# Performance work log

Hardware: AMD Instinct MI355X
Metric: run time of the kernel (lower is better)

## Reference

```python
import jax, jax.numpy as jnp
import numpy as np

GROUPS = 16
EPS_GN = 1e-6
EPS_L2 = 1e-12


def setup_inputs() -> dict:
    key = jax.random.key(0)
    ks = jax.random.split(key, 5)
    B, C, H, W = 8, 256, 64, 64
    s = 0.02
    return {
        "x": jax.random.normal(ks[0], (B, C, H, W), dtype=jnp.float32),
        "gn_gamma": jnp.ones((C,), dtype=jnp.float32),
        "gn_beta": jnp.zeros((C,), dtype=jnp.float32),
        "qkv_w": jax.random.normal(ks[1], (3 * C, C), dtype=jnp.float32) * s,
        "qkv_b": jax.random.normal(ks[2], (3 * C,), dtype=jnp.float32) * s,
        "temperature": jnp.ones((1, 1, 1), dtype=jnp.float32),  # (num_heads,1,1)
        "proj_w": jax.random.normal(ks[3], (C, C), dtype=jnp.float32) * s,
        "proj_b": jax.random.normal(ks[4], (C,), dtype=jnp.float32) * s,
    }


def _group_norm(x, gamma, beta):
    B, C, H, W = x.shape
    xg = x.reshape(B, GROUPS, C // GROUPS, H, W)
    mu = xg.mean(axis=(2, 3, 4), keepdims=True)
    var = xg.var(axis=(2, 3, 4), keepdims=True)
    xn = ((xg - mu) * jax.lax.rsqrt(var + EPS_GN)).reshape(B, C, H, W)
    return xn * gamma[None, :, None, None] + beta[None, :, None, None]


def _l2norm(t):
    # normalize along last axis (token axis N), matching F.normalize eps semantics
    n = jnp.sqrt(jnp.sum(t * t, axis=-1, keepdims=True))
    return t / jnp.maximum(n, EPS_L2)


def reference(x, gn_gamma, gn_beta, qkv_w, qkv_b, temperature, proj_w, proj_b):
    B, C, H, W = x.shape
    N = H * W
    nh = 1
    dh = C // nh

    h = _group_norm(x, gn_gamma, gn_beta).reshape(B, C, N).transpose(0, 2, 1)  # (B,N,C)

    qkv = h @ qkv_w.T + qkv_b                                   # (B,N,3C)
    qkv = qkv.reshape(B, N, 3, nh, dh).transpose(2, 0, 3, 4, 1)  # (3,B,nh,dh,N)
    q, k, v = qkv[0], qkv[1], qkv[2]

    q = _l2norm(q)
    k = _l2norm(k)

    # channel cross-covariance attention: (B,nh,dh,dh)
    attn = jax.nn.softmax(jnp.einsum('bhcn,bhdn->bhcd', q, k) * temperature[None], axis=-1)
    out = jnp.einsum('bhcd,bhdn->bhcn', attn, v)                 # (B,nh,dh,N)
    out = out.transpose(0, 3, 1, 2).reshape(B, N, C)             # (B,N,C)
    out = out @ proj_w.T + proj_b

    return x + out.transpose(0, 2, 1).reshape(B, C, H, W)
```

## Files before the change

### kernel.cpp

```cpp
#include <hip/hip_runtime.h>
#include <hip/hip_bf16.h>

namespace {

constexpr float EPS_GN = 1e-6f;
constexpr float EPS_L2 = 1e-12f;

typedef __attribute__((ext_vector_type(8))) short bf16x8;
typedef __attribute__((ext_vector_type(4))) float f32x4;

__device__ __forceinline__ unsigned short f2bf(float f) {
  union { __hip_bfloat16 h; unsigned short u; } cv;
  cv.h = __float2bfloat16(f);
  return cv.u;
}
__device__ __forceinline__ float blo(unsigned u) { return __uint_as_float(u << 16); }
__device__ __forceinline__ float bhi(unsigned u) { return __uint_as_float(u & 0xffff0000u); }

__global__ __launch_bounds__(256) void prep_k(const float* __restrict__ x,
                                              const float* __restrict__ qkv_w,
                                              const float* __restrict__ proj_w,
                                              unsigned short* __restrict__ xbf,
                                              unsigned short* __restrict__ xT,
                                              float* __restrict__ sxpart,
                                              unsigned short* __restrict__ qkvw_bf,
                                              unsigned short* __restrict__ pw_bf,
                                              unsigned short* __restrict__ wvt_bf) {
  __shared__ char shm[16640];
  const int bid = blockIdx.x, t = threadIdx.x;
  if (bid < 2048) {
    unsigned short (*tl)[68] = (unsigned short (*)[68])shm;
    const int b = bid >> 8, cy = (bid >> 6) & 3, nx = bid & 63;
    const int c0 = cy * 64, n0 = nx * 64;
    const int cl = t >> 2, ns = (t & 3) * 16;
    const float* xp = x + ((size_t)b << 20) + (size_t)(c0 + cl) * 4096 + n0 + ns;
    unsigned pk[8];
    float s = 0.f;
#pragma unroll
    for (int q = 0; q < 4; ++q) {
      float4 v = *(const float4*)(xp + q * 4);
      s += v.x + v.y + v.z + v.w;
      pk[2 * q + 0] = f2bf(v.x) | ((unsigned)f2bf(v.y) << 16);
      pk[2 * q + 1] = f2bf(v.z) | ((unsigned)f2bf(v.w) << 16);
    }
    unsigned short* xo = xbf + ((size_t)b << 20) + (size_t)(c0 + cl) * 4096 + n0 + ns;
    *(int4*)xo = make_int4((int)pk[0], (int)pk[1], (int)pk[2], (int)pk[3]);
    *(int4*)(xo + 8) = make_int4((int)pk[4], (int)pk[5], (int)pk[6], (int)pk[7]);
#pragma unroll
    for (int q = 0; q < 8; ++q)
      *(unsigned*)(&tl[cl][ns + 2 * q]) = pk[q];
    s += __shfl_xor(s, 1);
    s += __shfl_xor(s, 2);
    if ((t & 3) == 0)
      sxpart[((size_t)((b * 4 + cy) * 64 + cl)) * 64 + nx] = s;
    __syncthreads();
    const int nl = t >> 2, cs2 = (t & 3) * 16;
    unsigned pk2[8];
#pragma unroll
    for (int q = 0; q < 8; ++q)
      pk2[q] = (unsigned)(unsigned short)tl[cs2 + 2 * q][nl] |
               ((unsigned)(unsigned short)tl[cs2 + 2 * q + 1][nl] << 16);
    unsigned short* to = xT + ((size_t)((b << 12) + n0 + nl)) * 256 + c0 + cs2;
    *(int4*)to = make_int4((int)pk2[0], (int)pk2[1], (int)pk2[2], (int)pk2[3]);
    *(int4*)(to + 8) = make_int4((int)pk2[4], (int)pk2[5], (int)pk2[6], (int)pk2[7]);
    return;
  }
  const int cb = bid - 2048;
  if (cb < 256) {
    const float* src = (cb < 192) ? qkv_w : proj_w;
    unsigned short* dst = (cb < 192) ? qkvw_bf : pw_bf;
    int i = (cb < 192 ? cb : cb - 192) * 256 + t;
    float4 v = ((const float4*)src)[i];
    unsigned p0 = f2bf(v.x) | ((unsigned)f2bf(v.y) << 16);
    unsigned p1 = f2bf(v.z) | ((unsigned)f2bf(v.w) << 16);
    ((int2*)dst)[i] = make_int2((int)p0, (int)p1);
    return;
  }
  float (*tlf)[65] = (float (*)[65])shm;
  const int tb = cb - 256;
  const int j0 = (tb >> 2) * 64, d0 = (tb & 3) * 64;
  const float* src = qkv_w + 512 * 256;
  const int jr = t >> 2, ds = (t & 3) * 16;
#pragma unroll
  for (int q = 0; q < 4; ++q) {
    float4 v = *(const float4*)(src + (size_t)(j0 + jr) * 256 + d0 + ds + q * 4);
    tlf[jr][ds + q * 4 + 0] = v.x; tlf[jr][ds + q * 4 + 1] = v.y;
    tlf[jr][ds + q * 4 + 2] = v.z; tlf[jr][ds + q * 4 + 3] = v.w;
  }
  __syncthreads();
  const int dr = t >> 2, js = (t & 3) * 16;
  unsigned pk[8];
#pragma unroll
  for (int q = 0; q < 8; ++q)
    pk[q] = f2bf(tlf[js + 2 * q][dr]) | ((unsigned)f2bf(tlf[js + 2 * q + 1][dr]) << 16);
  unsigned short* dp = wvt_bf + (size_t)(d0 + dr) * 256 + j0 + js;
  *(int4*)dp = make_int4((int)pk[0], (int)pk[1], (int)pk[2], (int)pk[3]);
  *(int4*)(dp + 8) = make_int4((int)pk[4], (int)pk[5], (int)pk[6], (int)pk[7]);
}

#define NT64_BODY(APTR, ALDA, BPTR, BLDB, KSTEPS)                                   \
  const int tid = threadIdx.x;                                                      \
  const int l = tid & 63, w = tid >> 6;                                             \
  const int wm = w >> 1, wn = w & 1;                                                \
  const int r = tid >> 2;                                                           \
  const unsigned short* aG = (APTR) + (size_t)(m0 + r) * (ALDA) + (tid & 3) * 16;   \
  const unsigned short* bG = (BPTR) + (size_t)(n0 + r) * (BLDB) + (tid & 3) * 16;   \
  const int g0 = (tid & 3) * 2;                                                     \
  const int w0 = r * 128 + (((g0)     ^ (r & 7)) << 4);                             \
  const int w1 = r * 128 + (((g0 + 1) ^ (r & 7)) << 4);                             \
  int rdA[2], rdB[2];                                                               \
  _Pragma("unroll")                                                                 \
  for (int i = 0; i < 2; ++i) {                                                     \
    int rm = wm * 32 + i * 16 + (l & 15);                                           \
    rdA[i] = rm * 128 + (((l >> 4) ^ (rm & 7)) << 4);                               \
    int rn = wn * 32 + i * 16 + (l & 15);                                           \
    rdB[i] = rn * 128 + (((l >> 4) ^ (rn & 7)) << 4);                               \
  }                                                                                 \
  f32x4 zero = {0.f, 0.f, 0.f, 0.f};                                                \
  f32x4 acc[2][2] = {{zero, zero}, {zero, zero}};                                   \
  for (int ks = 0; ks < (KSTEPS); ++ks) {                                           \
    int4 a0 = *(const int4*)aG, a1 = *(const int4*)(aG + 8);                        \
    int4 b0 = *(const int4*)bG, b1 = *(const int4*)(bG + 8);                        \
    aG += 64; bG += 64;                                                             \
    __syncthreads();                                                                \
    *(int4*)((char*)As + w0) = a0; *(int4*)((char*)As + w1) = a1;                   \
    *(int4*)((char*)Bs + w0) = b0; *(int4*)((char*)Bs + w1) = b1;                   \
    __syncthreads();                                                                \
    _Pragma("unroll")                                                               \
    for (int kk = 0; kk < 2; ++kk) {                                                \
      bf16x8 af[2], bf_[2];                                                         \
      _Pragma("unroll")                                                             \
      for (int i = 0; i < 2; ++i) {                                                 \
        af[i]  = *(const bf16x8*)((const char*)As + (rdA[i] ^ (kk << 6)));          \
        bf_[i] = *(const bf16x8*)((const char*)Bs + (rdB[i] ^ (kk << 6)));          \
      }                                                                             \
      _Pragma("unroll")                                                             \
      for (int i = 0; i < 2; ++i)                                                   \
        _Pragma("unroll")                                                           \
        for (int j = 0; j < 2; ++j)                                                 \
          acc[i][j] = __builtin_amdgcn_mfma_f32_16x16x32_bf16(af[i], bf_[j],        \
                                                              acc[i][j], 0, 0, 0); \
    }                                                                               \
  }                                                                                 \
  const int mB = m0 + wm * 32 + ((l >> 4) << 2);                                    \
  const int nB = n0 + wn * 32 + (l & 15);

__global__ __launch_bounds__(256) void sxx64_k(const unsigned short* __restrict__ xbf,
                                               float* __restrict__ part) {
  __shared__ unsigned short As[4096];
  __shared__ unsigned short Bs[4096];
  const int z = blockIdx.z;
  const int b = z >> 3, sl = z & 7;
  const int m0 = blockIdx.y << 6, n0 = blockIdx.x << 6;
  const unsigned short* base = xbf + ((size_t)b << 20) + (size_t)sl * 512;
  NT64_BODY(base, 4096, base, 4096, 8)
  float* po = part + ((size_t)z << 16);
#pragma unroll
  for (int i = 0; i < 2; ++i)
#pragma unroll
    for (int rr = 0; rr < 4; ++rr)
#pragma unroll
      for (int j = 0; j < 2; ++j)
        po[(size_t)(mB + i * 16 + rr) * 256 + nB + j * 16] = acc[i][j][rr];
}

__global__ __launch_bounds__(256) void out64_k(const unsigned short* __restrict__ Fbf,
                                               const unsigned short* __restrict__ xT,
                                               const float* __restrict__ hvec,
                                               float* __restrict__ outF) {
  __shared__ unsigned short As[4096];
  __shared__ unsigned short Bs[4096];
  const int b = blockIdx.z;
  const int m0 = blockIdx.y << 6, n0 = blockIdx.x << 6;
  NT64_BODY(Fbf + ((size_t)b << 16), 256, xT + ((size_t)b << 20), 256, 4)
#pragma unroll
  for (int i = 0; i < 2; ++i) {
#pragma unroll
    for (int rr = 0; rr < 4; ++rr) {
      int mi = mB + i * 16 + rr;
      float hv = hvec[b * 256 + mi];
      size_t rowo = ((size_t)b << 20) + (size_t)mi * 4096;
#pragma unroll
      for (int j = 0; j < 2; ++j)
        outF[rowo + nB + j * 16] = acc[i][j][rr] + hv;
    }
  }
}

__global__ __launch_bounds__(256) void gfill2_k(const float* __restrict__ part,
                                                const float* __restrict__ sxpart,
                                                const float* __restrict__ gamma,
                                                const float* __restrict__ beta,
                                                const unsigned short* __restrict__ qkvw_bf,
                                                float* __restrict__ avec,
                                                float* __restrict__ evec,
                                                float* __restrict__ wsv,
                                                unsigned short* __restrict__ Gbf) {
  __shared__ float sav[256], sev[256], ssx[256], ssv[256];
  const int b = blockIdx.y, t = threadIdx.x;

  {
    const float* sp = sxpart + ((size_t)(b * 256 + t) << 6);
    float sxv = 0.f;
#pragma unroll 4
    for (int i = 0; i < 64; ++i) sxv += sp[i];
    float dg = 0.f;
#pragma unroll
    for (int s = 0; s < 8; ++s) dg += part[((size_t)(b * 8 + s) << 16) + t * 257];
    float gs = sxv, g2 = dg;
#pragma unroll
    for (int off = 1; off < 16; off <<= 1) {
      gs += __shfl_xor(gs, off);
      g2 += __shfl_xor(g2, off);
    }
    const float inv = 1.f / 65536.f;
    float mu = gs * inv;
    float var = g2 * inv - mu * mu;
    float rstd = rsqrtf(var + EPS_GN);
    float av = gamma[t] * rstd;
    float ev = beta[t] - mu * av;
    sav[t] = av; sev[t] = ev; ssx[t] = sxv;
    ssv[t] = av * sxv + 4096.f * ev;
    if (blockIdx.x == 0) {
      avec[b * 256 + t] = av;
      evec[b * 256 + t] = ev;
    }
  }
  __syncthreads();

  {
    const int row = blockIdx.x * 32 + (t >> 3);
    const int seg = (t & 7) * 32;
    const unsigned short* wr = qkvw_bf + (size_t)row * 256 + seg;
    float acc = 0.f;
#pragma unroll
    for (int d = 0; d < 32; d += 8) {
      int4 v = *(const int4*)(wr + d);
      acc += blo((unsigned)v.x) * ssv[seg + d + 0] + bhi((unsigned)v.x) * ssv[seg + d + 1];
      acc += blo((unsigned)v.y) * ssv[seg + d + 2] + bhi((unsigned)v.y) * ssv[seg + d + 3];
      acc += blo((unsigned)v.z) * ssv[seg + d + 4] + bhi((unsigned)v.z) * ssv[seg + d + 5];
      acc += blo((unsigned)v.w) * ssv[seg + d + 6] + bhi((unsigned)v.w) * ssv[seg + d + 7];
    }
    acc += __shfl_xor(acc, 1);
    acc += __shfl_xor(acc, 2);
    acc += __shfl_xor(acc, 4);
    if ((t & 7) == 0) wsv[b * 512 + row] = acc;
  }

  {
    const int rr_ = blockIdx.x * 16 + (t >> 4);
    const int cs = (t & 15) * 16;
    const float ac = sav[rr_], ec = sev[rr_], sxc = ssx[rr_];
    unsigned pk[8];
#pragma unroll
    for (int q = 0; q < 8; ++q) {
      unsigned lohi[2];
#pragma unroll
      for (int h = 0; h < 2; ++h) {
        int d = cs + 2 * q + h;
        float S = 0.f;
#pragma unroll
        for (int s = 0; s < 8; ++s)
          S += part[(((size_t)(b * 8 + s)) << 16) + (size_t)rr_ * 256 + d];
        float gv = ac * sav[d] * S + ac * sev[d] * sxc + ec * sav[d] * ssx[d] +
                   4096.f * ec * sev[d];
        lohi[h] = f2bf(gv);
      }
      pk[q] = lohi[0] | (lohi[1] << 16);
    }
    unsigned short* gp = Gbf + ((size_t)b << 16) + (size_t)rr_ * 256 + cs;
    *(int4*)gp = make_int4((int)pk[0], (int)pk[1], (int)pk[2], (int)pk[3]);
    *(int4*)(gp + 8) = make_int4((int)pk[4], (int)pk[5], (int)pk[6], (int)pk[7]);
  }
}

__global__ __launch_bounds__(256) void ugemm_k(const unsigned short* __restrict__ qkvw,
                                               const unsigned short* __restrict__ Gbf,
                                               unsigned short* __restrict__ Ubf) {
  __shared__ unsigned short As[4096];
  __shared__ unsigned short Bs[4096];
  const int b = blockIdx.z;
  const int m0 = blockIdx.y << 6, n0 = blockIdx.x << 6;
  NT64_BODY(qkvw, 256, Gbf + ((size_t)b << 16), 256, 4)
  unsigned short* pu = Ubf + ((size_t)b << 17);
#pragma unroll
  for (int i = 0; i < 2; ++i)
#pragma unroll
    for (int rr = 0; rr < 4; ++rr)
#pragma unroll
      for (int j = 0; j < 2; ++j)
        pu[(size_t)(mB + i * 16 + rr) * 256 + nB + j * 16] = f2bf(acc[i][j][rr]);
}

__global__ __launch_bounds__(256) void y1h_k(const unsigned short* __restrict__ wvt,
                                             const unsigned short* __restrict__ Abf,
                                             const float* __restrict__ abv,
                                             const float* __restrict__ proj_w,
                                             const float* __restrict__ proj_b,
                                             unsigned short* __restrict__ Y1,
                                             float* __restrict__ hvec) {
  __shared__ unsigned short As[4096];
  __shared__ unsigned short Bs[4096];
  __shared__ float abl[256];
  const int b = blockIdx.z;
  const int m0 = blockIdx.y << 6, n0 = blockIdx.x << 6;
  NT64_BODY(wvt, 256, Abf + ((size_t)b << 16), 256, 4)
  unsigned short* pu = Y1 + ((size_t)b << 16);
#pragma unroll
  for (int i = 0; i < 2; ++i)
#pragma unroll
    for (int rr = 0; rr < 4; ++rr)
#pragma unroll
      for (int j = 0; j < 2; ++j)
        pu[(size_t)(mB + i * 16 + rr) * 256 + nB + j * 16] = f2bf(acc[i][j][rr]);
  if (blockIdx.y == 0) {
    abl[tid] = abv[b * 256 + tid];
    __syncthreads();
    const int t = n0 + (tid >> 2);
    const int qd = (tid & 3) * 64;
    const float* pr = proj_w + (size_t)t * 256 + qd;
    float s = 0.f;
#pragma unroll 8
    for (int i = 0; i < 64; ++i) s += pr[i] * abl[qd + i];
    s += __shfl_xor(s, 1);
    s += __shfl_xor(s, 2);
    if ((tid & 3) == 0) hvec[b * 256 + t] = proj_b[t] + s;
  }
}

__global__ __launch_bounds__(256) void fgen_k(const unsigned short* __restrict__ pw,
                                              const unsigned short* __restrict__ Y1,
                                              const float* __restrict__ avec,
                                              const float* __restrict__ evec,
                                              unsigned short* __restrict__ Fbf,
                                              float* __restrict__ hvec) {
  __shared__ unsigned short As[4096];
  __shared__ unsigned short Bs[4096];
  const int b = blockIdx.z;
  const int m0 = blockIdx.y << 6, n0 = blockIdx.x << 6;
  NT64_BODY(pw, 256, Y1 + ((size_t)b << 16), 256, 4)
  __syncthreads();
  float* hred = (float*)As;
  if (tid < 64) hred[tid] = 0.f;
  __syncthreads();
#pragma unroll
  for (int i = 0; i < 2; ++i) {
#pragma unroll
    for (int rr = 0; rr < 4; ++rr) {
      int t = mB + i * 16 + rr;
      float hp = 0.f;
#pragma unroll
      for (int j = 0; j < 2; ++j) {
        int d = nB + j * 16;
        float f = acc[i][j][rr];
        float fa = f * avec[b * 256 + d] + (t == d ? 1.f : 0.f);
        Fbf[((size_t)b << 16) + (size_t)t * 256 + d] = f2bf(fa);
        hp += f * evec[b * 256 + d];
      }
      atomicAdd(&hred[t - m0], hp);
    }
  }
  __syncthreads();
  if (tid < 64) atomicAdd(&hvec[b * 256 + m0 + tid], hred[tid]);
}

__global__ __launch_bounds__(256) void logsm_k(
    const unsigned short* __restrict__ Ubf,
    const unsigned short* __restrict__ qkvw,
    const float* __restrict__ wsv,
    const float* __restrict__ qkv_b, const float* __restrict__ temp,
    unsigned short* __restrict__ Abf, float* __restrict__ abv) {
  __shared__ unsigned short As[64 * 64];
  __shared__ unsigned short Bs[256 * 64];
  const int b = blockIdx.y, m0 = blockIdx.x * 64;
  const int tid = threadIdx.x;
  const int l = tid & 63, w = tid >> 6;
  const unsigned short* wk = qkvw + 65536;

  const int ar = tid >> 2, ac = tid & 3;
  const unsigned short* aG = Ubf + ((size_t)b << 17) + (size_t)(m0 + ar) * 256 + ac * 16;
  const unsigned short* bG = wk + (size_t)tid * 256;
  const int g0 = ac * 2;
  const int wA0 = ar * 128 + (((g0)     ^ (ar & 7)) << 4);
  const int wA1 = ar * 128 + (((g0 + 1) ^ (ar & 7)) << 4);
  int wBoff[8];
#pragma unroll
  for (int c = 0; c < 8; ++c) wBoff[c] = tid * 128 + ((c ^ (tid & 7)) << 4);

  int rdA;
  { int rm = w * 16 + (l & 15); rdA = rm * 128 + (((l >> 4) ^ (rm & 7)) << 4); }
  int rdB[16];
#pragma unroll
  for (int nf = 0; nf < 16; ++nf) {
    int rn = nf * 16 + (l & 15);
    rdB[nf] = rn * 128 + (((l >> 4) ^ (rn & 7)) << 4);
  }

  f32x4 zero = {0.f, 0.f, 0.f, 0.f};
  f32x4 acc[16];
#pragma unroll
  for (int nf = 0; nf < 16; ++nf) acc[nf] = zero;

  for (int ks = 0; ks < 4; ++ks) {
    int4 a0 = *(const int4*)aG;
    int4 a1 = *(const int4*)(aG + 8);
    int4 bv[8];
#pragma unroll
    for (int c = 0; c < 8; ++c) bv[c] = *(const int4*)(bG + c * 8);
    aG += 64; bG += 64;
    __syncthreads();
    *(int4*)((char*)As + wA0) = a0;
    *(int4*)((char*)As + wA1) = a1;
#pragma unroll
    for (int c = 0; c < 8; ++c) *(int4*)((char*)Bs + wBoff[c]) = bv[c];
    __syncthreads();
#pragma unroll
    for (int kk = 0; kk < 2; ++kk) {
      bf16x8 af = *(const bf16x8*)((const char*)As + (rdA ^ (kk << 6)));
#pragma unroll
      for (int nf = 0; nf < 16; ++nf) {
        bf16x8 bf_ = *(const bf16x8*)((const char*)Bs + (rdB[nf] ^ (kk << 6)));
        acc[nf] = __builtin_amdgcn_mfma_f32_16x16x32_bf16(af, bf_, acc[nf], 0, 0, 0);
      }
    }
  }

  __syncthreads();
  float* sKs  = (float*)As;
  float* sWks = sKs + 256;
  float* sBk  = sWks + 256;
  float* sBv  = sBk + 256;
  float* sQs  = sBv + 256;
  {
    const unsigned short* ur = Ubf + ((size_t)b << 17) + (size_t)(256 + tid) * 256;
    const unsigned short* wr = wk + (size_t)tid * 256;
    float dot = 0.f;
    for (int dd = 0; dd < 256; dd += 8) {
      int4 uv = *(const int4*)(ur + dd);
      int4 wv = *(const int4*)(wr + dd);
      dot += blo((unsigned)uv.x) * blo((unsigned)wv.x) + bhi((unsigned)uv.x) * bhi((unsigned)wv.x);
      dot += blo((unsigned)uv.y) * blo((unsigned)wv.y) + bhi((unsigned)uv.y) * bhi((unsigned)wv.y);
      dot += blo((unsigned)uv.z) * blo((unsigned)wv.z) + bhi((unsigned)uv.z) * bhi((unsigned)wv.z);
      dot += blo((unsigned)uv.w) * blo((unsigned)wv.w) + bhi((unsigned)uv.w) * bhi((unsigned)wv.w);
    }
    float bk = qkv_b[256 + tid];
    float wks = wsv[b * 512 + 256 + tid];
    float n2 = dot + 2.f * bk * wks + 4096.f * bk * bk;
    sKs[tid]  = 1.f / fmaxf(sqrtf(fmaxf(n2, 0.f)), EPS_L2);
    sWks[tid] = wks;
    sBk[tid]  = bk;
    sBv[tid]  = qkv_b[512 + tid];
  }
  if (tid < 64) {
    int m = m0 + tid;
    const unsigned short* ur = Ubf + ((size_t)b << 17) + (size_t)m * 256;
    const unsigned short* wr = qkvw + (size_t)m * 256;
    float dot = 0.f;
    for (int dd = 0; dd < 256; dd += 8) {
      int4 uv = *(const int4*)(ur + dd);
      int4 wv = *(const int4*)(wr + dd);
      dot += blo((unsigned)uv.x) * blo((unsigned)wv.x) + bhi((unsigned)uv.x) * bhi((unsigned)wv.x);
      dot += blo((unsigned)uv.y) * blo((unsigned)wv.y) + bhi((unsigned)uv.y) * bhi((unsigned)wv.y);
      dot += blo((unsigned)uv.z) * blo((unsigned)wv.z) + bhi((unsigned)uv.z) * bhi((unsigned)wv.z);
      dot += blo((unsigned)uv.w) * blo((unsigned)wv.w) + bhi((unsigned)uv.w) * bhi((unsigned)wv.w);
    }
    float bq = qkv_b[m], wqs = wsv[b * 512 + m];
    float n2 = dot + 2.f * bq * wqs + 4096.f * bq * bq;
    sQs[tid] = 1.f / fmaxf(sqrtf(fmaxf(n2, 0.f)), EPS_L2);
  }
  __syncthreads();

  const float T = temp[0];
  const int lrow = w * 16 + ((l >> 4) << 2);
  const int mrow = m0 + lrow;
  float ks_c[16], wks_c[16], bk_c[16], bv_c[16];
#pragma unroll
  for (int nf = 0; nf < 16; ++nf) {
    int n = nf * 16 + (l & 15);
    ks_c[nf] = sKs[n]; wks_c[nf] = sWks[n]; bk_c[nf] = sBk[n]; bv_c[nf] = sBv[n];
  }
#pragma unroll
  for (int rr = 0; rr < 4; ++rr) {
    int m = mrow + rr;
    float qs = sQs[lrow + rr], wqs = wsv[b * 512 + m], bq = qkv_b[m];
    float sc = T * qs;
#pragma unroll
    for (int nf = 0; nf < 16; ++nf)
      acc[nf][rr] = sc * ks_c[nf] *
                    (acc[nf][rr] + bq * wks_c[nf] + bk_c[nf] * wqs + 4096.f * bq * bk_c[nf]);
    float mx = acc[0][rr];
#pragma unroll
    for (int nf = 1; nf < 16; ++nf) mx = fmaxf(mx, acc[nf][rr]);
    mx = fmaxf(mx, __shfl_xor(mx, 1));
    mx = fmaxf(mx, __shfl_xor(mx, 2));
    mx = fmaxf(mx, __shfl_xor(mx, 4));
    mx = fmaxf(mx, __shfl_xor(mx, 8));
    float s = 0.f, ab = 0.f;
#pragma unroll
    for (int nf = 0; nf < 16; ++nf) {
      float e = __expf(acc[nf][rr] - mx);
      acc[nf][rr] = e;
      s += e; ab += e * bv_c[nf];
    }
#pragma unroll
    for (int off = 1; off < 16; off <<= 1) {
      s += __shfl_xor(s, off);
      ab += __shfl_xor(ab, off);
    }
    float inv = 1.f / s;
    unsigned short* arow = Abf + ((size_t)b << 16) + (size_t)m * 256 + (l & 15);
#pragma unroll
    for (int nf = 0; nf < 16; ++nf)
      arow[nf * 16] = f2bf(acc[nf][rr] * inv);
    if ((l & 15) == 0) abv[b * 256 + m] = ab * inv;
  }
}

}

extern "C" void kernel_launch(void* const* d_in, const int* in_sizes, int n_in,
                              void* d_out, int out_size, void* d_ws, size_t ws_size,
                              hipStream_t stream) {
  const float* x      = (const float*)d_in[0];
  const float* gamma  = (const float*)d_in[1];
  const float* beta   = (const float*)d_in[2];
  const float* qkv_w  = (const float*)d_in[3];
  const float* qkv_b  = (const float*)d_in[4];
  const float* temp   = (const float*)d_in[5];
  const float* proj_w = (const float*)d_in[6];
  const float* proj_b = (const float*)d_in[7];
  float* out = (float*)d_out;

  char* ws = (char*)d_ws;
  const size_t MB = 1048576;
  unsigned short* qkvw_bf = (unsigned short*)(ws);
  unsigned short* pw_bf   = (unsigned short*)(ws + 0x60000);
  unsigned short* wvt_bf  = (unsigned short*)(ws + 0x80000);
  float* avec  = (float*)(ws + 0xA0000);
  float* evec  = (float*)(ws + 0xA2000);
  float* wsv   = (float*)(ws + 0xA6000);
  float* hvec  = (float*)(ws + 0xAA000);
  float* abv   = (float*)(ws + 0xAC000);
  float* sxpart = (float*)(ws + 1 * MB);
  float* part   = (float*)(ws + 2 * MB);
  unsigned short* Gbf = (unsigned short*)(ws + 18 * MB);
  unsigned short* Ubf = (unsigned short*)(ws + 19 * MB);
  unsigned short* Abf = (unsigned short*)(ws + 21 * MB);
  unsigned short* Y1  = (unsigned short*)(ws + 22 * MB);
  unsigned short* Fbf = (unsigned short*)(ws + 23 * MB);
  unsigned short* xbf = (unsigned short*)(ws + 24 * MB);
  unsigned short* xT  = (unsigned short*)(ws + 40 * MB);
  if (ws_size < 56 * MB) return;

  prep_k<<<2320, 256, 0, stream>>>(x, qkv_w, proj_w, xbf, xT, sxpart,
                                   qkvw_bf, pw_bf, wvt_bf);

  sxx64_k<<<dim3(4, 4, 64), 256, 0, stream>>>(xbf, part);

  gfill2_k<<<dim3(16, 8), 256, 0, stream>>>(part, sxpart, gamma, beta, qkvw_bf,
                                            avec, evec, wsv, Gbf);

  ugemm_k<<<dim3(4, 8, 8), 256, 0, stream>>>(qkvw_bf, Gbf, Ubf);

  logsm_k<<<dim3(4, 8), 256, 0, stream>>>(Ubf, qkvw_bf, wsv, qkv_b, temp, Abf, abv);

  y1h_k<<<dim3(4, 4, 8), 256, 0, stream>>>(wvt_bf, Abf, abv, proj_w, proj_b, Y1, hvec);

  fgen_k<<<dim3(4, 4, 8), 256, 0, stream>>>(pw_bf, Y1, avec, evec, Fbf, hvec);

  out64_k<<<dim3(64, 4, 8), 256, 0, stream>>>(Fbf, xT, hvec, out);
}
```

Measured before the change: 106.9 us.

## Fuse Y1 and F generation GEMMs into one kernel with LDS-resident Y1

Merges the y1h and fgen kernels into a single kernel. Each block computes a 64-column strip of Y1 (all 256 rows) into LDS, then multiplies it by the proj-weight tile to produce F. hvec is now zeroed in gfill2 and accumulated with atomics from both contributions. This removes a kernel launch and the global round trip of Y1, at the cost of redundant Y1 computation (each d-strip is recomputed by every t0 block) and a larger LDS footprint.

```diff
diff --git a/kernel.cpp b/kernel.cpp
--- a/kernel.cpp
+++ b/kernel.cpp
@@ -195,6 +195,7 @@
                                                 float* __restrict__ avec,
                                                 float* __restrict__ evec,
                                                 float* __restrict__ wsv,
+                                                float* __restrict__ hvec,
                                                 unsigned short* __restrict__ Gbf) {
   __shared__ float sav[256], sev[256], ssx[256], ssv[256];
   const int b = blockIdx.y, t = threadIdx.x;
@@ -224,6 +225,7 @@
     if (blockIdx.x == 0) {
       avec[b * 256 + t] = av;
       evec[b * 256 + t] = ev;
+      hvec[b * 256 + t] = 0.f;
     }
   }
   __syncthreads();
@@ -292,31 +294,137 @@
         pu[(size_t)(mB + i * 16 + rr) * 256 + nB + j * 16] = f2bf(acc[i][j][rr]);
 }
 
-__global__ __launch_bounds__(256) void y1h_k(const unsigned short* __restrict__ wvt,
-                                             const unsigned short* __restrict__ Abf,
-                                             const float* __restrict__ abv,
-                                             const float* __restrict__ proj_w,
-                                             const float* __restrict__ proj_b,
-                                             unsigned short* __restrict__ Y1,
-                                             float* __restrict__ hvec) {
+__global__ __launch_bounds__(256) void fgen2_k(const unsigned short* __restrict__ wvt,
+                                               const unsigned short* __restrict__ Abf,
+                                               const unsigned short* __restrict__ pw,
+                                               const float* __restrict__ abv,
+                                               const float* __restrict__ proj_w,
+                                               const float* __restrict__ proj_b,
+                                               const float* __restrict__ avec,
+                                               const float* __restrict__ evec,
+                                               unsigned short* __restrict__ Fbf,
+                                               float* __restrict__ hvec) {
   __shared__ unsigned short As[4096];
   __shared__ unsigned short Bs[4096];
-  __shared__ float abl[256];
+  __shared__ unsigned short Ylds[16384];
   const int b = blockIdx.z;
-  const int m0 = blockIdx.y << 6, n0 = blockIdx.x << 6;
-  NT64_BODY(wvt, 256, Abf + ((size_t)b << 16), 256, 4)
-  unsigned short* pu = Y1 + ((size_t)b << 16);
-#pragma unroll
-  for (int i = 0; i < 2; ++i)
-#pragma unroll
-    for (int rr = 0; rr < 4; ++rr)
-#pragma unroll
-      for (int j = 0; j < 2; ++j)
-        pu[(size_t)(mB + i * 16 + rr) * 256 + nB + j * 16] = f2bf(acc[i][j][rr]);
-  if (blockIdx.y == 0) {
-    abl[tid] = abv[b * 256 + tid];
-    __syncthreads();
-    const int t = n0 + (tid >> 2);
+  const int d0 = blockIdx.x << 6;
+  const int t0 = blockIdx.y << 6;
+  const int tid = threadIdx.x;
+  const int l = tid & 63, w = tid >> 6;
+  const int wm = w >> 1, wn = w & 1;
+  const int r = tid >> 2;
+  const int g0 = (tid & 3) * 2;
+  const int w0 = r * 128 + ((g0 ^ (r & 7)) << 4);
+  const int w1 = r * 128 + (((g0 + 1) ^ (r & 7)) << 4);
+  int rdA[2], rdB[2];
+#pragma unroll
+  for (int i = 0; i < 2; ++i) {
+    int rm = wm * 32 + i * 16 + (l & 15);
+    rdA[i] = rm * 128 + (((l >> 4) ^ (rm & 7)) << 4);
+    int rn = wn * 32 + i * 16 + (l & 15);
+    rdB[i] = rn * 128 + (((l >> 4) ^ (rn & 7)) << 4);
+  }
+  const int mloc = wm * 32 + ((l >> 4) << 2);
+  const int nloc = wn * 32 + (l & 15);
+  f32x4 zero = {0.f, 0.f, 0.f, 0.f};
+
+  for (int ni = 0; ni < 4; ++ni) {
+    const unsigned short* aG = wvt + (size_t)(d0 + r) * 256 + (tid & 3) * 16;
+    const unsigned short* bG = Abf + ((size_t)b << 16) + (size_t)(ni * 64 + r) * 256 + (tid & 3) * 16;
+    f32x4 acc[2][2] = {{zero, zero}, {zero, zero}};
+    for (int ks = 0; ks < 4; ++ks) {
+      int4 a0 = *(const int4*)aG, a1 = *(const int4*)(aG + 8);
+      int4 b0 = *(const int4*)bG, b1 = *(const int4*)(bG + 8);
+      aG += 64; bG += 64;
+      __syncthreads();
+      *(int4*)((char*)As + w0) = a0; *(int4*)((char*)As + w1) = a1;
+      *(int4*)((char*)Bs + w0) = b0; *(int4*)((char*)Bs + w1) = b1;
+      __syncthreads();
+#pragma unroll
+      for (int kk = 0; kk < 2; ++kk) {
+        bf16x8 af[2], bf_[2];
+#pragma unroll
+        for (int i = 0; i < 2; ++i) {
+          af[i]  = *(const bf16x8*)((const char*)As + (rdA[i] ^ (kk << 6)));
+          bf_[i] = *(const bf16x8*)((const char*)Bs + (rdB[i] ^ (kk << 6)));
+        }
+#pragma unroll
+        for (int i = 0; i < 2; ++i)
+#pragma unroll
+          for (int j = 0; j < 2; ++j)
+            acc[i][j] = __builtin_amdgcn_mfma_f32_16x16x32_bf16(af[i], bf_[j], acc[i][j], 0, 0, 0);
+      }
+    }
+#pragma unroll
+    for (int i = 0; i < 2; ++i) {
+#pragma unroll
+      for (int rr = 0; rr < 4; ++rr) {
+        int dl = mloc + i * 16 + rr;
+#pragma unroll
+        for (int j = 0; j < 2; ++j) {
+          int kl = nloc + j * 16;
+          int byte = ni * 8192 + dl * 128 + (((kl >> 3) ^ (dl & 7)) << 4) + (kl & 7) * 2;
+          *(unsigned short*)((char*)Ylds + byte) = f2bf(acc[i][j][rr]);
+        }
+      }
+    }
+  }
+  __syncthreads();
+
+  f32x4 acc2[2][2] = {{zero, zero}, {zero, zero}};
+  {
+    const unsigned short* aG = pw + (size_t)(t0 + r) * 256 + (tid & 3) * 16;
+    for (int ks = 0; ks < 4; ++ks) {
+      int4 a0 = *(const int4*)aG, a1 = *(const int4*)(aG + 8);
+      aG += 64;
+      __syncthreads();
+      *(int4*)((char*)As + w0) = a0; *(int4*)((char*)As + w1) = a1;
+      __syncthreads();
+#pragma unroll
+      for (int kk = 0; kk < 2; ++kk) {
+        bf16x8 af[2], bf_[2];
+#pragma unroll
+        for (int i = 0; i < 2; ++i) {
+          af[i]  = *(const bf16x8*)((const char*)As + (rdA[i] ^ (kk << 6)));
+          bf_[i] = *(const bf16x8*)((const char*)Ylds + ks * 8192 + (rdB[i] ^ (kk << 6)));
+        }
+#pragma unroll
+        for (int i = 0; i < 2; ++i)
+#pragma unroll
+          for (int j = 0; j < 2; ++j)
+            acc2[i][j] = __builtin_amdgcn_mfma_f32_16x16x32_bf16(af[i], bf_[j], acc2[i][j], 0, 0, 0);
+      }
+    }
+  }
+
+  float* hred = (float*)Bs;
+  float* abl  = (float*)((char*)Bs + 1024);
+  if (tid < 64) hred[tid] = 0.f;
+  if (d0 == 0) abl[tid] = abv[b * 256 + tid];
+  __syncthreads();
+#pragma unroll
+  for (int i = 0; i < 2; ++i) {
+#pragma unroll
+    for (int rr = 0; rr < 4; ++rr) {
+      int tl_ = mloc + i * 16 + rr;
+      int t = t0 + tl_;
+      float hp = 0.f;
+#pragma unroll
+      for (int j = 0; j < 2; ++j) {
+        int d = d0 + nloc + j * 16;
+        float f = acc2[i][j][rr];
+        float fa = f * avec[b * 256 + d] + (t == d ? 1.f : 0.f);
+        Fbf[((size_t)b << 16) + (size_t)t * 256 + d] = f2bf(fa);
+        hp += f * evec[b * 256 + d];
+      }
+      atomicAdd(&hred[tl_], hp);
+    }
+  }
+  __syncthreads();
+  if (tid < 64) atomicAdd(&hvec[b * 256 + t0 + tid], hred[tid]);
+  if (d0 == 0) {
+    const int t = t0 + (tid >> 2);
     const int qd = (tid & 3) * 64;
     const float* pr = proj_w + (size_t)t * 256 + qd;
     float s = 0.f;
@@ -324,44 +432,8 @@
     for (int i = 0; i < 64; ++i) s += pr[i] * abl[qd + i];
     s += __shfl_xor(s, 1);
     s += __shfl_xor(s, 2);
-    if ((tid & 3) == 0) hvec[b * 256 + t] = proj_b[t] + s;
-  }
-}
-
-__global__ __launch_bounds__(256) void fgen_k(const unsigned short* __restrict__ pw,
-                                              const unsigned short* __restrict__ Y1,
-                                              const float* __restrict__ avec,
-                                              const float* __restrict__ evec,
-                                              unsigned short* __restrict__ Fbf,
-                                              float* __restrict__ hvec) {
-  __shared__ unsigned short As[4096];
-  __shared__ unsigned short Bs[4096];
-  const int b = blockIdx.z;
-  const int m0 = blockIdx.y << 6, n0 = blockIdx.x << 6;
-  NT64_BODY(pw, 256, Y1 + ((size_t)b << 16), 256, 4)
-  __syncthreads();
-  float* hred = (float*)As;
-  if (tid < 64) hred[tid] = 0.f;
-  __syncthreads();
-#pragma unroll
-  for (int i = 0; i < 2; ++i) {
-#pragma unroll
-    for (int rr = 0; rr < 4; ++rr) {
-      int t = mB + i * 16 + rr;
-      float hp = 0.f;
-#pragma unroll
-      for (int j = 0; j < 2; ++j) {
-        int d = nB + j * 16;
-        float f = acc[i][j][rr];
-        float fa = f * avec[b * 256 + d] + (t == d ? 1.f : 0.f);
-        Fbf[((size_t)b << 16) + (size_t)t * 256 + d] = f2bf(fa);
-        hp += f * evec[b * 256 + d];
-      }
-      atomicAdd(&hred[t - m0], hp);
-    }
-  }
-  __syncthreads();
-  if (tid < 64) atomicAdd(&hvec[b * 256 + m0 + tid], hred[tid]);
+    if ((tid & 3) == 0) atomicAdd(&hvec[b * 256 + t], proj_b[t] + s);
+  }
 }
 
 __global__ __launch_bounds__(256) void logsm_k(
@@ -546,7 +618,6 @@
   unsigned short* Gbf = (unsigned short*)(ws + 18 * MB);
   unsigned short* Ubf = (unsigned short*)(ws + 19 * MB);
   unsigned short* Abf = (unsigned short*)(ws + 21 * MB);
-  unsigned short* Y1  = (unsigned short*)(ws + 22 * MB);
   unsigned short* Fbf = (unsigned short*)(ws + 23 * MB);
   unsigned short* xbf = (unsigned short*)(ws + 24 * MB);
   unsigned short* xT  = (unsigned short*)(ws + 40 * MB);
@@ -558,15 +629,14 @@
   sxx64_k<<<dim3(4, 4, 64), 256, 0, stream>>>(xbf, part);
 
   gfill2_k<<<dim3(16, 8), 256, 0, stream>>>(part, sxpart, gamma, beta, qkvw_bf,
-                                            avec, evec, wsv, Gbf);
+                                            avec, evec, wsv, hvec, Gbf);
 
   ugemm_k<<<dim3(4, 8, 8), 256, 0, stream>>>(qkvw_bf, Gbf, Ubf);
 
   logsm_k<<<dim3(4, 8), 256, 0, stream>>>(Ubf, qkvw_bf, wsv, qkv_b, temp, Abf, abv);
 
-  y1h_k<<<dim3(4, 4, 8), 256, 0, stream>>>(wvt_bf, Abf, abv, proj_w, proj_b, Y1, hvec);
-
-  fgen_k<<<dim3(4, 4, 8), 256, 0, stream>>>(pw_bf, Y1, avec, evec, Fbf, hvec);
+  fgen2_k<<<dim3(4, 4, 8), 256, 0, stream>>>(wvt_bf, Abf, pw_bf, abv, proj_w, proj_b,
+                                             avec, evec, Fbf, hvec);
 
   out64_k<<<dim3(64, 4, 8), 256, 0, stream>>>(Fbf, xT, hvec, out);
 }
```

Result: slower. 111.9 us (+4.7%).

## Fuse Gram-matrix fill into the U GEMM kernel via shared memory

Applied to the files above, without the earlier changes.

Merges the gfill2 kernel (which reduces partial Gram sums, applies group-norm affine correction and writes a bf16 G matrix to global) into the ugemm kernel. Each block now builds its 64-column slice of G directly in a swizzled shared-memory buffer and runs the MFMA GEMM against it, so one launch and the G round trip through global memory go away. The cost is that every m-tile block (8 per column tile) recomputes the same G slice and group-norm stats from the 8 partial buffers, which adds redundant global reads and ALU work. It also uses more LDS per block.

```diff
diff --git a/kernel.cpp b/kernel.cpp
--- a/kernel.cpp
+++ b/kernel.cpp
@@ -187,26 +187,45 @@
   }
 }
 
-__global__ __launch_bounds__(256) void gfill2_k(const float* __restrict__ part,
-                                                const float* __restrict__ sxpart,
-                                                const float* __restrict__ gamma,
-                                                const float* __restrict__ beta,
-                                                const unsigned short* __restrict__ qkvw_bf,
-                                                float* __restrict__ avec,
-                                                float* __restrict__ evec,
-                                                float* __restrict__ wsv,
-                                                unsigned short* __restrict__ Gbf) {
+__global__ __launch_bounds__(256) void gu_k(const float* __restrict__ part,
+                                            const float* __restrict__ sxpart,
+                                            const float* __restrict__ gamma,
+                                            const float* __restrict__ beta,
+                                            const unsigned short* __restrict__ qkvw,
+                                            float* __restrict__ avec,
+                                            float* __restrict__ evec,
+                                            float* __restrict__ wsv,
+                                            unsigned short* __restrict__ Ubf) {
+  __shared__ unsigned short As[4096];
+  __shared__ unsigned short Gs[16384];
   __shared__ float sav[256], sev[256], ssx[256], ssv[256];
-  const int b = blockIdx.y, t = threadIdx.x;
+  const int b = blockIdx.z;
+  const int n0 = blockIdx.x << 6;
+  const int m0 = blockIdx.y << 6;
+  const int tid = threadIdx.x;
+  const int l = tid & 63, w = tid >> 6;
+  const int wm = w >> 1, wn = w & 1;
+  const int r = tid >> 2;
+  const int g0 = (tid & 3) * 2;
+  const int w0 = r * 128 + ((g0 ^ (r & 7)) << 4);
+  const int w1 = r * 128 + (((g0 + 1) ^ (r & 7)) << 4);
+  int rdA[2], rdB[2];
+#pragma unroll
+  for (int i = 0; i < 2; ++i) {
+    int rm = wm * 32 + i * 16 + (l & 15);
+    rdA[i] = rm * 128 + (((l >> 4) ^ (rm & 7)) << 4);
+    int rn = wn * 32 + i * 16 + (l & 15);
+    rdB[i] = rn * 128 + (((l >> 4) ^ (rn & 7)) << 4);
+  }
 
   {
-    const float* sp = sxpart + ((size_t)(b * 256 + t) << 6);
+    const float* sp = sxpart + ((size_t)(b * 256 + tid) << 6);
     float sxv = 0.f;
 #pragma unroll 4
     for (int i = 0; i < 64; ++i) sxv += sp[i];
     float dg = 0.f;
 #pragma unroll
-    for (int s = 0; s < 8; ++s) dg += part[((size_t)(b * 8 + s) << 16) + t * 257];
+    for (int s = 0; s < 8; ++s) dg += part[((size_t)(b * 8 + s) << 16) + tid * 257];
     float gs = sxv, g2 = dg;
 #pragma unroll
     for (int off = 1; off < 16; off <<= 1) {
@@ -217,24 +236,24 @@
     float mu = gs * inv;
     float var = g2 * inv - mu * mu;
     float rstd = rsqrtf(var + EPS_GN);
-    float av = gamma[t] * rstd;
-    float ev = beta[t] - mu * av;
-    sav[t] = av; sev[t] = ev; ssx[t] = sxv;
-    ssv[t] = av * sxv + 4096.f * ev;
-    if (blockIdx.x == 0) {
-      avec[b * 256 + t] = av;
-      evec[b * 256 + t] = ev;
-    }
-  }
-  __syncthreads();
-
-  {
-    const int row = blockIdx.x * 32 + (t >> 3);
-    const int seg = (t & 7) * 32;
-    const unsigned short* wr = qkvw_bf + (size_t)row * 256 + seg;
+    float av = gamma[tid] * rstd;
+    float ev = beta[tid] - mu * av;
+    sav[tid] = av; sev[tid] = ev; ssx[tid] = sxv;
+    ssv[tid] = av * sxv + 4096.f * ev;
+    if (blockIdx.x == 0 && blockIdx.y == 0) {
+      avec[b * 256 + tid] = av;
+      evec[b * 256 + tid] = ev;
+    }
+  }
+  __syncthreads();
+
+  if (blockIdx.x == 0) {
+    const int row = m0 + (tid >> 2);
+    const int seg = (tid & 3) * 64;
+    const unsigned short* wr = qkvw + (size_t)row * 256 + seg;
     float acc = 0.f;
 #pragma unroll
-    for (int d = 0; d < 32; d += 8) {
+    for (int d = 0; d < 64; d += 8) {
       int4 v = *(const int4*)(wr + d);
       acc += blo((unsigned)v.x) * ssv[seg + d + 0] + bhi((unsigned)v.x) * ssv[seg + d + 1];
       acc += blo((unsigned)v.y) * ssv[seg + d + 2] + bhi((unsigned)v.y) * ssv[seg + d + 3];
@@ -243,45 +262,77 @@
     }
     acc += __shfl_xor(acc, 1);
     acc += __shfl_xor(acc, 2);
-    acc += __shfl_xor(acc, 4);
-    if ((t & 7) == 0) wsv[b * 512 + row] = acc;
+    if ((tid & 3) == 0) wsv[b * 512 + row] = acc;
   }
 
   {
-    const int rr_ = blockIdx.x * 16 + (t >> 4);
-    const int cs = (t & 15) * 16;
-    const float ac = sav[rr_], ec = sev[rr_], sxc = ssx[rr_];
-    unsigned pk[8];
-#pragma unroll
-    for (int q = 0; q < 8; ++q) {
-      unsigned lohi[2];
-#pragma unroll
-      for (int h = 0; h < 2; ++h) {
-        int d = cs + 2 * q + h;
-        float S = 0.f;
-#pragma unroll
-        for (int s = 0; s < 8; ++s)
-          S += part[(((size_t)(b * 8 + s)) << 16) + (size_t)rr_ * 256 + d];
-        float gv = ac * sav[d] * S + ac * sev[d] * sxc + ec * sav[d] * ssx[d] +
-                   4096.f * ec * sev[d];
-        lohi[h] = f2bf(gv);
+    const int rl = tid >> 4;
+    const int ds0 = (tid & 15) * 16;
+    const int ksbuf = ds0 >> 6;
+    const int kl0 = ds0 & 63;
+    for (int sub = 0; sub < 4; ++sub) {
+      const int row_local = sub * 16 + rl;
+      const int c = n0 + row_local;
+      const float ac = sav[c], ec = sev[c], sxc = ssx[c];
+      float S[16];
+#pragma unroll
+      for (int q = 0; q < 16; ++q) S[q] = 0.f;
+      for (int s = 0; s < 8; ++s) {
+        const float* pp = part + (((size_t)(b * 8 + s)) << 16) + (size_t)c * 256 + ds0;
+#pragma unroll
+        for (int q4 = 0; q4 < 4; ++q4) {
+          float4 v = *(const float4*)(pp + q4 * 4);
+          S[q4 * 4 + 0] += v.x; S[q4 * 4 + 1] += v.y;
+          S[q4 * 4 + 2] += v.z; S[q4 * 4 + 3] += v.w;
+        }
       }
-      pk[q] = lohi[0] | (lohi[1] << 16);
-    }
-    unsigned short* gp = Gbf + ((size_t)b << 16) + (size_t)rr_ * 256 + cs;
-    *(int4*)gp = make_int4((int)pk[0], (int)pk[1], (int)pk[2], (int)pk[3]);
-    *(int4*)(gp + 8) = make_int4((int)pk[4], (int)pk[5], (int)pk[6], (int)pk[7]);
-  }
-}
-
-__global__ __launch_bounds__(256) void ugemm_k(const unsigned short* __restrict__ qkvw,
-                                               const unsigned short* __restrict__ Gbf,
-                                               unsigned short* __restrict__ Ubf) {
-  __shared__ unsigned short As[4096];
-  __shared__ unsigned short Bs[4096];
-  const int b = blockIdx.z;
-  const int m0 = blockIdx.y << 6, n0 = blockIdx.x << 6;
-  NT64_BODY(qkvw, 256, Gbf + ((size_t)b << 16), 256, 4)
+      unsigned pk[8];
+#pragma unroll
+      for (int q = 0; q < 8; ++q) {
+        int d0_ = ds0 + 2 * q, d1_ = ds0 + 2 * q + 1;
+        float gv0 = ac * sav[d0_] * S[2 * q]     + ac * sev[d0_] * sxc +
+                    ec * sav[d0_] * ssx[d0_]     + 4096.f * ec * sev[d0_];
+        float gv1 = ac * sav[d1_] * S[2 * q + 1] + ac * sev[d1_] * sxc +
+                    ec * sav[d1_] * ssx[d1_]     + 4096.f * ec * sev[d1_];
+        pk[q] = f2bf(gv0) | ((unsigned)f2bf(gv1) << 16);
+      }
+      const int base = ksbuf * 8192 + row_local * 128;
+      const int slot0 = base + ((((kl0 >> 3) + 0) ^ (row_local & 7)) << 4);
+      const int slot1 = base + ((((kl0 >> 3) + 1) ^ (row_local & 7)) << 4);
+      *(int4*)((char*)Gs + slot0) = make_int4((int)pk[0], (int)pk[1], (int)pk[2], (int)pk[3]);
+      *(int4*)((char*)Gs + slot1) = make_int4((int)pk[4], (int)pk[5], (int)pk[6], (int)pk[7]);
+    }
+  }
+  __syncthreads();
+
+  f32x4 zero = {0.f, 0.f, 0.f, 0.f};
+  f32x4 acc2[2][2] = {{zero, zero}, {zero, zero}};
+  {
+    const unsigned short* aG = qkvw + (size_t)(m0 + r) * 256 + (tid & 3) * 16;
+    for (int ks = 0; ks < 4; ++ks) {
+      int4 a0 = *(const int4*)aG, a1 = *(const int4*)(aG + 8);
+      aG += 64;
+      __syncthreads();
+      *(int4*)((char*)As + w0) = a0; *(int4*)((char*)As + w1) = a1;
+      __syncthreads();
+#pragma unroll
+      for (int kk = 0; kk < 2; ++kk) {
+        bf16x8 af[2], bf_[2];
+#pragma unroll
+        for (int i = 0; i < 2; ++i) {
+          af[i]  = *(const bf16x8*)((const char*)As + (rdA[i] ^ (kk << 6)));
+          bf_[i] = *(const bf16x8*)((const char*)Gs + ks * 8192 + (rdB[i] ^ (kk << 6)));
+        }
+#pragma unroll
+        for (int i = 0; i < 2; ++i)
+#pragma unroll
+          for (int j = 0; j < 2; ++j)
+            acc2[i][j] = __builtin_amdgcn_mfma_f32_16x16x32_bf16(af[i], bf_[j], acc2[i][j], 0, 0, 0);
+      }
+    }
+  }
+  const int mB = m0 + wm * 32 + ((l >> 4) << 2);
+  const int nB = n0 + wn * 32 + (l & 15);
   unsigned short* pu = Ubf + ((size_t)b << 17);
 #pragma unroll
   for (int i = 0; i < 2; ++i)
@@ -289,7 +340,7 @@
     for (int rr = 0; rr < 4; ++rr)
 #pragma unroll
       for (int j = 0; j < 2; ++j)
-        pu[(size_t)(mB + i * 16 + rr) * 256 + nB + j * 16] = f2bf(acc[i][j][rr]);
+        pu[(size_t)(mB + i * 16 + rr) * 256 + nB + j * 16] = f2bf(acc2[i][j][rr]);
 }
 
 __global__ __launch_bounds__(256) void y1h_k(const unsigned short* __restrict__ wvt,
@@ -543,7 +594,6 @@
   float* abv   = (float*)(ws + 0xAC000);
   float* sxpart = (float*)(ws + 1 * MB);
   float* part   = (float*)(ws + 2 * MB);
-  unsigned short* Gbf = (unsigned short*)(ws + 18 * MB);
   unsigned short* Ubf = (unsigned short*)(ws + 19 * MB);
   unsigned short* Abf = (unsigned short*)(ws + 21 * MB);
   unsigned short* Y1  = (unsigned short*)(ws + 22 * MB);
@@ -557,10 +607,8 @@
 
   sxx64_k<<<dim3(4, 4, 64), 256, 0, stream>>>(xbf, part);
 
-  gfill2_k<<<dim3(16, 8), 256, 0, stream>>>(part, sxpart, gamma, beta, qkvw_bf,
-                                            avec, evec, wsv, Gbf);
-
-  ugemm_k<<<dim3(4, 8, 8), 256, 0, stream>>>(qkvw_bf, Gbf, Ubf);
+  gu_k<<<dim3(4, 8, 8), 256, 0, stream>>>(part, sxpart, gamma, beta, qkvw_bf,
+                                          avec, evec, wsv, Ubf);
 
   logsm_k<<<dim3(4, 8), 256, 0, stream>>>(Ubf, qkvw_bf, wsv, qkv_b, temp, Abf, abv);
 
```

New measurement: 110.1 us. 3.0% more time.
